# Performance work log

Hardware: AMD Instinct MI355X
Metric: run time of the kernel (lower is better)

The kernel has to match this reference:

```python
import jax, jax.numpy as jnp
import numpy as np

EMBED_DIM = 1024
NUM_HEADS = 16
HEAD_DIM = EMBED_DIM // NUM_HEADS


def setup_inputs() -> dict:
    key = jax.random.key(0)
    ks = jax.random.split(key, 9)
    s = 1.0 / np.sqrt(EMBED_DIM)
    inp = {"x": jax.random.normal(ks[0], (4, 8192, EMBED_DIM), dtype=jnp.float32)}
    for i, name in enumerate(["q", "k", "v", "o"]):
        inp[f"W{name}"] = jax.random.uniform(ks[1 + 2 * i], (EMBED_DIM, EMBED_DIM), jnp.float32, -s, s)
        inp[f"b{name}"] = jax.random.uniform(ks[2 + 2 * i], (EMBED_DIM,), jnp.float32, -s, s)
    return inp


def _kernel_exp(x):
    # exp(x - max over last dim), matches torch exp kernel
    return jnp.exp(x - jnp.max(x, axis=-1, keepdims=True))


def reference(x, Wq, bq, Wk, bk, Wv, bv, Wo, bo):
    b, s, e = x.shape
    def proj(W, bias):
        # (b,s,e) -> (b,h,s,d)
        return (x @ W.T + bias).reshape(b, s, NUM_HEADS, HEAD_DIM).transpose(0, 2, 1, 3)
    q = proj(Wq, bq)
    k = proj(Wk, bk)
    v = proj(Wv, bv)
    q_kern = _kernel_exp(q)
    k_kern = _kernel_exp(k)
    # global KV reduction: kv[b,h,d,e'] = sum_s k_kern[b,h,s,d] v[b,h,s,e']
    kv = jnp.einsum('bhsd,bhse->bhde', k_kern, v)
    # denom[b,h,q] = sum_{s,d} q_kern[b,h,q,d] k_kern[b,h,s,d] = q_kern . k_sum
    k_sum = jnp.sum(k_kern, axis=2)  # (b,h,d)
    denom = jnp.einsum('bhqd,bhd->bhq', q_kern, k_sum) + 1e-6
    y = jnp.einsum('bhqd,bhde->bhqe', q_kern, kv) / denom[..., None]
    y = y.transpose(0, 2, 1, 3).reshape(b, s, e)
    return y @ Wo.T + bo
```

## Files before the change

### kernel.cpp

```cpp
#include <hip/hip_runtime.h>
#include <hip/hip_bf16.h>
#include <cstdint>
#include <cstddef>


#define B_ 4
#define S_ 8192
#define E_ 1024
#define H_ 16
#define D_ 64
#define M_ (B_ * S_)

typedef __attribute__((ext_vector_type(8))) short s16x8;
typedef __attribute__((ext_vector_type(4))) short s16x4;
typedef __attribute__((ext_vector_type(4))) float f32x4_t;

__device__ __forceinline__ float bf2f(unsigned short u) {
  union { unsigned int i; float f; } c; c.i = ((unsigned int)u) << 16; return c.f;
}
__device__ __forceinline__ short f2bf(float f) {
  __hip_bfloat16 h = __float2bfloat16(f);
  return *reinterpret_cast<short*>(&h);
}

__global__ __launch_bounds__(256) void f32_to_bf16(
    const float* __restrict__ in, unsigned short* __restrict__ out, long n8)
{
  const long i = (long)blockIdx.x * 256 + threadIdx.x;
  if (i >= n8) return;
  const float4 lo = *(const float4*)(in + i * 8);
  const float4 hi = *(const float4*)(in + i * 8 + 4);
  s16x8 v;
  v[0] = f2bf(lo.x); v[1] = f2bf(lo.y); v[2] = f2bf(lo.z); v[3] = f2bf(lo.w);
  v[4] = f2bf(hi.x); v[5] = f2bf(hi.y); v[6] = f2bf(hi.z); v[7] = f2bf(hi.w);
  *(s16x8*)(out + i * 8) = v;
}

__device__ __forceinline__ void gload_lds16(const void* g, void* l) {
  __builtin_amdgcn_global_load_lds(
      (const __attribute__((address_space(1))) void*)g,
      (__attribute__((address_space(3))) void*)l, 16, 0, 0);
}

template <bool OUT_BF16>
__global__ __launch_bounds__(256) void gemm_bf16(
    const unsigned short* __restrict__ Xb,
    const unsigned short* __restrict__ Wb,
    const float* __restrict__ bias,
    void* __restrict__ Cout,
    int M, int N, int K)
{
  __shared__ unsigned short Al[128 * 64];
  __shared__ unsigned short Bl[128 * 64];
  const int tid = threadIdx.x;
  const int lane = tid & 63, w = tid >> 6;
  const int nwg = gridDim.x;
  const int cpx = nwg >> 3;
  const int swz = (blockIdx.x & 7) * cpx + (blockIdx.x >> 3);
  const int ntx = N >> 7;
  const int m0 = (swz / ntx) << 7, n0 = (swz % ntx) << 7;
  const int wr = w >> 1, wc = w & 1;
  const int srow = lane >> 3;
  const int scol = (lane & 7) * 8;
  const int fr = lane & 15, fq = lane >> 4;

  f32x4_t acc[4][4];
  #pragma unroll
  for (int i = 0; i < 4; ++i)
    #pragma unroll
    for (int j = 0; j < 4; ++j) acc[i][j] = (f32x4_t){0.f, 0.f, 0.f, 0.f};

  for (int kt = 0; kt < K; kt += 64) {
    #pragma unroll
    for (int i = 0; i < 4; ++i) {
      const int c = w * 4 + i;
      const int row = c * 8 + srow;
      gload_lds16(Xb + (size_t)(m0 + row) * K + kt + scol, Al + c * 512);
      gload_lds16(Wb + (size_t)(n0 + row) * K + kt + scol, Bl + c * 512);
    }
    asm volatile("s_waitcnt vmcnt(0)" ::: "memory");
    __syncthreads();
    #pragma unroll
    for (int ks = 0; ks < 2; ++ks) {
      s16x8 a[4], b[4];
      #pragma unroll
      for (int mi = 0; mi < 4; ++mi)
        a[mi] = *(const s16x8*)(Al + (wr * 64 + mi * 16 + fr) * 64 + ks * 32 + fq * 8);
      #pragma unroll
      for (int ni = 0; ni < 4; ++ni)
        b[ni] = *(const s16x8*)(Bl + (wc * 64 + ni * 16 + fr) * 64 + ks * 32 + fq * 8);
      #pragma unroll
      for (int mi = 0; mi < 4; ++mi)
        #pragma unroll
        for (int ni = 0; ni < 4; ++ni)
          acc[mi][ni] = __builtin_amdgcn_mfma_f32_16x16x32_bf16(a[mi], b[ni], acc[mi][ni], 0, 0, 0);
    }
    __syncthreads();
  }

  #pragma unroll
  for (int ni = 0; ni < 4; ++ni) {
    const int col = n0 + wc * 64 + ni * 16 + fr;
    const float bcol = bias[col];
    #pragma unroll
    for (int mi = 0; mi < 4; ++mi)
      #pragma unroll
      for (int r = 0; r < 4; ++r) {
        const int row = m0 + wr * 64 + mi * 16 + fq * 4 + r;
        const float v = acc[mi][ni][r] + bcol;
        if (OUT_BF16)
          ((unsigned short*)Cout)[(size_t)row * N + col] = (unsigned short)f2bf(v);
        else
          ((float*)Cout)[(size_t)row * N + col] = v;
      }
  }
}

#define NCHUNK 16
#define CROWS (S_ / NCHUNK)
#define KVR 8

__global__ __launch_bounds__(256) void kv_partial(
    const unsigned short* __restrict__ Kb, const unsigned short* __restrict__ Vb,
    float* __restrict__ kv_part, float* __restrict__ ksum_part)
{
  const int chunk = blockIdx.x;
  const int bh = blockIdx.y;
  const int b = bh >> 4, h = bh & 15;
  const int tid = threadIdx.x;
  const int lane = tid & 63, wave = tid >> 6;
  const int tx = tid & 15, ty = tid >> 4;

  __shared__ float kl[KVR][64];
  __shared__ float vl[KVR][64];
  __shared__ float ksw[4][64];

  const size_t base = ((size_t)b * S_ + (size_t)chunk * CROWS) * E_ + h * D_;
  const unsigned short* kbase = Kb + base;
  const unsigned short* vbase = Vb + base;

  float acc[4][4] = {};
  float ksacc = 0.f;

  const int which = tid >> 7;
  const int l2 = tid & 127;
  const int lr = l2 >> 4;
  const int lc = (l2 & 15) * 4;

  for (int s = 0; s < CROWS; s += KVR) {
    {
      const unsigned short* src = which ? vbase : kbase;
      float* dst = which ? &vl[lr][lc] : &kl[lr][lc];
      const s16x4 raw = *(const s16x4*)(src + (size_t)(s + lr) * E_ + lc);
      dst[0] = bf2f((unsigned short)raw[0]);
      dst[1] = bf2f((unsigned short)raw[1]);
      dst[2] = bf2f((unsigned short)raw[2]);
      dst[3] = bf2f((unsigned short)raw[3]);
    }
    __syncthreads();
    #pragma unroll
    for (int rr = 0; rr < 2; ++rr) {
      const int r = wave * 2 + rr;
      const float kx = kl[r][lane];
      float mx = kx;
      #pragma unroll
      for (int off = 32; off >= 1; off >>= 1) mx = fmaxf(mx, __shfl_xor(mx, off, 64));
      const float e = expf(kx - mx);
      kl[r][lane] = e;
      ksacc += e;
    }
    __syncthreads();
    #pragma unroll
    for (int r = 0; r < KVR; ++r) {
      const float4 kd = *(const float4*)&kl[r][ty * 4];
      const float4 ve = *(const float4*)&vl[r][tx * 4];
      const float kda[4] = {kd.x, kd.y, kd.z, kd.w};
      const float vea[4] = {ve.x, ve.y, ve.z, ve.w};
      #pragma unroll
      for (int i = 0; i < 4; ++i)
        #pragma unroll
        for (int j = 0; j < 4; ++j)
          acc[i][j] = fmaf(kda[i], vea[j], acc[i][j]);
    }
    __syncthreads();
  }

  const size_t pbase = ((size_t)bh * NCHUNK + chunk) * (D_ * D_);
  #pragma unroll
  for (int i = 0; i < 4; ++i) {
    float4 o = make_float4(acc[i][0], acc[i][1], acc[i][2], acc[i][3]);
    *(float4*)(kv_part + pbase + (size_t)(ty * 4 + i) * D_ + tx * 4) = o;
  }
  ksw[wave][lane] = ksacc;
  __syncthreads();
  if (wave == 0) {
    const float s = ksw[0][lane] + ksw[1][lane] + ksw[2][lane] + ksw[3][lane];
    ksum_part[((size_t)bh * NCHUNK + chunk) * D_ + lane] = s;
  }
}

__global__ __launch_bounds__(256) void kv_reduce(
    const float* __restrict__ kv_part, const float* __restrict__ ksum_part,
    float* __restrict__ kv, float* __restrict__ ksum)
{
  const int bh = blockIdx.x;
  const int tid = threadIdx.x;
  #pragma unroll
  for (int i = 0; i < 16; ++i) {
    const int e = tid + i * 256;
    float s = 0.f;
    #pragma unroll
    for (int c = 0; c < NCHUNK; ++c)
      s += kv_part[((size_t)bh * NCHUNK + c) * 4096 + e];
    kv[(size_t)bh * 4096 + e] = s;
  }
  if (tid < 64) {
    float s = 0.f;
    #pragma unroll
    for (int c = 0; c < NCHUNK; ++c)
      s += ksum_part[((size_t)bh * NCHUNK + c) * 64 + tid];
    ksum[(size_t)bh * 64 + tid] = s;
  }
}

__global__ __launch_bounds__(256) void y_kernel(
    const unsigned short* __restrict__ Qb, const float* __restrict__ kv,
    const float* __restrict__ ksum, unsigned short* __restrict__ Yb)
{
  const int tile = blockIdx.x;
  const int bh = blockIdx.y;
  const int b = bh >> 4, h = bh & 15;
  const int tid = threadIdx.x;
  const int lane = tid & 63, wave = tid >> 6;
  const int tx = tid & 15, ty = tid >> 4;

  __shared__ float qT[64][65];
  __shared__ float kvl[64][64];
  __shared__ float ksl[64];
  __shared__ float dinv[64];

  #pragma unroll
  for (int i = 0; i < 4; ++i) {
    const int l = tid + i * 256;
    *(float4*)&((float*)kvl)[4 * l] = *(const float4*)(kv + (size_t)bh * 4096 + 4 * l);
  }
  if (tid < 64) ksl[tid] = ksum[(size_t)bh * 64 + tid];
  __syncthreads();

  const unsigned short* qbase = Qb + ((size_t)b * S_ + (size_t)tile * 64) * E_ + h * D_;
  for (int rr = 0; rr < 16; ++rr) {
    const int r = wave * 16 + rr;
    const float q = bf2f(qbase[(size_t)r * E_ + lane]);
    float mx = q;
    #pragma unroll
    for (int off = 32; off >= 1; off >>= 1) mx = fmaxf(mx, __shfl_xor(mx, off, 64));
    const float e = expf(q - mx);
    qT[lane][r] = e;
    float dp = e * ksl[lane];
    #pragma unroll
    for (int off = 32; off >= 1; off >>= 1) dp += __shfl_xor(dp, off, 64);
    if (lane == 0) dinv[r] = 1.f / (dp + 1e-6f);
  }
  __syncthreads();

  float acc[4][4] = {};
  #pragma unroll 8
  for (int kk = 0; kk < 64; ++kk) {
    const float4 a = *(const float4*)&qT[kk][ty * 4];
    const float4 v = *(const float4*)&kvl[kk][tx * 4];
    const float aa[4] = {a.x, a.y, a.z, a.w};
    const float vv[4] = {v.x, v.y, v.z, v.w};
    #pragma unroll
    for (int i = 0; i < 4; ++i)
      #pragma unroll
      for (int j = 0; j < 4; ++j)
        acc[i][j] = fmaf(aa[i], vv[j], acc[i][j]);
  }

  unsigned short* ybase = Yb + ((size_t)b * S_ + (size_t)tile * 64) * E_ + h * D_;
  #pragma unroll
  for (int i = 0; i < 4; ++i) {
    const int r = ty * 4 + i;
    const float sc = dinv[r];
    s16x4 o;
    o[0] = f2bf(acc[i][0] * sc); o[1] = f2bf(acc[i][1] * sc);
    o[2] = f2bf(acc[i][2] * sc); o[3] = f2bf(acc[i][3] * sc);
    *(s16x4*)(ybase + (size_t)r * E_ + tx * 4) = o;
  }
}

extern "C" void kernel_launch(void* const* d_in, const int* in_sizes, int n_in,
                              void* d_out, int out_size, void* d_ws, size_t ws_size,
                              hipStream_t stream)
{
  (void)in_sizes; (void)n_in; (void)out_size; (void)ws_size;
  const float* x  = (const float*)d_in[0];
  const float* Wq = (const float*)d_in[1];
  const float* bq = (const float*)d_in[2];
  const float* Wk = (const float*)d_in[3];
  const float* bk = (const float*)d_in[4];
  const float* Wv = (const float*)d_in[5];
  const float* bv = (const float*)d_in[6];
  const float* Wo = (const float*)d_in[7];
  const float* bo = (const float*)d_in[8];
  float* out = (float*)d_out;

  const size_t ME = (size_t)M_ * E_;
  const size_t EE = (size_t)E_ * E_;
  unsigned short* qb  = (unsigned short*)d_ws;
  unsigned short* kb  = qb + ME;
  unsigned short* vb  = kb + ME;
  unsigned short* xb  = vb + ME;
  unsigned short* wqb = xb + ME;
  unsigned short* wkb = wqb + EE;
  unsigned short* wvb = wkb + EE;
  unsigned short* wob = wvb + EE;
  float* kv_part  = (float*)(wob + EE);
  float* ksum_prt = kv_part + (size_t)64 * NCHUNK * 4096;
  float* kvb      = ksum_prt + (size_t)64 * NCHUNK * 64;
  float* ksum     = kvb + (size_t)64 * 4096;
  unsigned short* yb = xb;

  f32_to_bf16<<<(int)(ME / 8 / 256), 256, 0, stream>>>(x, xb, (long)(ME / 8));
  f32_to_bf16<<<(int)(EE / 8 / 256), 256, 0, stream>>>(Wq, wqb, (long)(EE / 8));
  f32_to_bf16<<<(int)(EE / 8 / 256), 256, 0, stream>>>(Wk, wkb, (long)(EE / 8));
  f32_to_bf16<<<(int)(EE / 8 / 256), 256, 0, stream>>>(Wv, wvb, (long)(EE / 8));
  f32_to_bf16<<<(int)(EE / 8 / 256), 256, 0, stream>>>(Wo, wob, (long)(EE / 8));

  const int nwg = (M_ / 128) * (E_ / 128);
  gemm_bf16<true><<<nwg, 256, 0, stream>>>(xb, wqb, bq, qb, M_, E_, E_);
  gemm_bf16<true><<<nwg, 256, 0, stream>>>(xb, wkb, bk, kb, M_, E_, E_);
  gemm_bf16<true><<<nwg, 256, 0, stream>>>(xb, wvb, bv, vb, M_, E_, E_);
  kv_partial<<<dim3(NCHUNK, 64), 256, 0, stream>>>(kb, vb, kv_part, ksum_prt);
  kv_reduce<<<dim3(64), 256, 0, stream>>>(kv_part, ksum_prt, kvb, ksum);
  y_kernel<<<dim3(S_ / 64, 64), 256, 0, stream>>>(qb, kvb, ksum, yb);
  gemm_bf16<false><<<nwg, 256, 0, stream>>>(yb, wob, bo, out, M_, E_, E_);
}
```

Measured before the change: 956.5 us.

## Fuse QKV GEMMs with exp epilogue, restage KV reduction, use MFMA for output

Merges the three projection GEMMs into one launch over a concatenated weight matrix. The per-head max/exp feature map for Q and K now runs in the GEMM epilogue, so the later kernels read exp'd values directly. The KV partial kernel stages 64-row tiles and drops its per-row exp, and the y kernel replaces its scalar FMA loop with bf16 MFMA against a transposed bf16 KV matrix. In exchange, the KV matrix is rounded to bf16, which adds precision loss.

```diff
diff --git a/kernel.cpp b/kernel.cpp
--- a/kernel.cpp
+++ b/kernel.cpp
@@ -42,14 +42,15 @@
       (__attribute__((address_space(3))) void*)l, 16, 0, 0);
 }
 
-template <bool OUT_BF16>
-__global__ __launch_bounds__(256) void gemm_bf16(
+__global__ __launch_bounds__(256) void gemm_qkv(
     const unsigned short* __restrict__ Xb,
-    const unsigned short* __restrict__ Wb,
-    const float* __restrict__ bias,
-    void* __restrict__ Cout,
-    int M, int N, int K)
-{
+    const unsigned short* __restrict__ Wcat,
+    const float* __restrict__ bq, const float* __restrict__ bk,
+    const float* __restrict__ bv,
+    unsigned short* __restrict__ qe, unsigned short* __restrict__ ke,
+    unsigned short* __restrict__ vb)
+{
+  const int K = E_, N = 3 * E_;
   __shared__ unsigned short Al[128 * 64];
   __shared__ unsigned short Bl[128 * 64];
   const int tid = threadIdx.x;
@@ -76,7 +77,7 @@
       const int c = w * 4 + i;
       const int row = c * 8 + srow;
       gload_lds16(Xb + (size_t)(m0 + row) * K + kt + scol, Al + c * 512);
-      gload_lds16(Wb + (size_t)(n0 + row) * K + kt + scol, Bl + c * 512);
+      gload_lds16(Wcat + (size_t)(n0 + row) * K + kt + scol, Bl + c * 512);
     }
     asm volatile("s_waitcnt vmcnt(0)" ::: "memory");
     __syncthreads();
@@ -98,82 +99,97 @@
     __syncthreads();
   }
 
+  const int c0 = n0 + wc * 64;
+  const int id = c0 >> 10;
+  const int lc0 = c0 & 1023;
+  const float* bias = (id == 0) ? bq : (id == 1) ? bk : bv;
+  unsigned short* outp = (id == 0) ? qe : (id == 1) ? ke : vb;
+
+  float val[4][4][4];
   #pragma unroll
   for (int ni = 0; ni < 4; ++ni) {
-    const int col = n0 + wc * 64 + ni * 16 + fr;
-    const float bcol = bias[col];
+    const float bcol = bias[lc0 + ni * 16 + fr];
+    #pragma unroll
+    for (int mi = 0; mi < 4; ++mi)
+      #pragma unroll
+      for (int r = 0; r < 4; ++r)
+        val[mi][ni][r] = acc[mi][ni][r] + bcol;
+  }
+
+  if (id < 2) {
+    #pragma unroll
+    for (int mi = 0; mi < 4; ++mi)
+      #pragma unroll
+      for (int r = 0; r < 4; ++r) {
+        float mx = fmaxf(fmaxf(val[mi][0][r], val[mi][1][r]),
+                         fmaxf(val[mi][2][r], val[mi][3][r]));
+        mx = fmaxf(mx, __shfl_xor(mx, 1));
+        mx = fmaxf(mx, __shfl_xor(mx, 2));
+        mx = fmaxf(mx, __shfl_xor(mx, 4));
+        mx = fmaxf(mx, __shfl_xor(mx, 8));
+        #pragma unroll
+        for (int ni = 0; ni < 4; ++ni)
+          val[mi][ni][r] = expf(val[mi][ni][r] - mx);
+      }
+  }
+
+  #pragma unroll
+  for (int ni = 0; ni < 4; ++ni) {
+    const int col = lc0 + ni * 16 + fr;
     #pragma unroll
     for (int mi = 0; mi < 4; ++mi)
       #pragma unroll
       for (int r = 0; r < 4; ++r) {
         const int row = m0 + wr * 64 + mi * 16 + fq * 4 + r;
-        const float v = acc[mi][ni][r] + bcol;
-        if (OUT_BF16)
-          ((unsigned short*)Cout)[(size_t)row * N + col] = (unsigned short)f2bf(v);
-        else
-          ((float*)Cout)[(size_t)row * N + col] = v;
+        outp[(size_t)row * E_ + col] = (unsigned short)f2bf(val[mi][ni][r]);
       }
   }
 }
 
 #define NCHUNK 16
 #define CROWS (S_ / NCHUNK)
-#define KVR 8
-
-__global__ __launch_bounds__(256) void kv_partial(
-    const unsigned short* __restrict__ Kb, const unsigned short* __restrict__ Vb,
+
+__global__ __launch_bounds__(256) void kv_core(
+    const unsigned short* __restrict__ Ke, const unsigned short* __restrict__ Vb,
     float* __restrict__ kv_part, float* __restrict__ ksum_part)
 {
   const int chunk = blockIdx.x;
   const int bh = blockIdx.y;
   const int b = bh >> 4, h = bh & 15;
   const int tid = threadIdx.x;
-  const int lane = tid & 63, wave = tid >> 6;
   const int tx = tid & 15, ty = tid >> 4;
 
-  __shared__ float kl[KVR][64];
-  __shared__ float vl[KVR][64];
-  __shared__ float ksw[4][64];
-
-  const size_t base = ((size_t)b * S_ + (size_t)chunk * CROWS) * E_ + h * D_;
-  const unsigned short* kbase = Kb + base;
-  const unsigned short* vbase = Vb + base;
+  __shared__ float kst[64][64];
+  __shared__ float vst[64][64];
+
+  const size_t rbase = ((size_t)b * S_ + (size_t)chunk * CROWS);
 
   float acc[4][4] = {};
-  float ksacc = 0.f;
-
-  const int which = tid >> 7;
-  const int l2 = tid & 127;
-  const int lr = l2 >> 4;
-  const int lc = (l2 & 15) * 4;
-
-  for (int s = 0; s < CROWS; s += KVR) {
+  float ksacc[4] = {0.f, 0.f, 0.f, 0.f};
+
+  const int lrow = tid >> 2;
+  const int lcq = (tid & 3) * 16;
+
+  for (int it = 0; it < CROWS / 64; ++it) {
     {
-      const unsigned short* src = which ? vbase : kbase;
-      float* dst = which ? &vl[lr][lc] : &kl[lr][lc];
-      const s16x4 raw = *(const s16x4*)(src + (size_t)(s + lr) * E_ + lc);
-      dst[0] = bf2f((unsigned short)raw[0]);
-      dst[1] = bf2f((unsigned short)raw[1]);
-      dst[2] = bf2f((unsigned short)raw[2]);
-      dst[3] = bf2f((unsigned short)raw[3]);
-    }
-    __syncthreads();
-    #pragma unroll
-    for (int rr = 0; rr < 2; ++rr) {
-      const int r = wave * 2 + rr;
-      const float kx = kl[r][lane];
-      float mx = kx;
-      #pragma unroll
-      for (int off = 32; off >= 1; off >>= 1) mx = fmaxf(mx, __shfl_xor(mx, off, 64));
-      const float e = expf(kx - mx);
-      kl[r][lane] = e;
-      ksacc += e;
-    }
-    __syncthreads();
-    #pragma unroll
-    for (int r = 0; r < KVR; ++r) {
-      const float4 kd = *(const float4*)&kl[r][ty * 4];
-      const float4 ve = *(const float4*)&vl[r][tx * 4];
+      const size_t g = (rbase + it * 64 + lrow) * E_ + h * D_ + lcq;
+      const s16x8 k0 = *(const s16x8*)(Ke + g);
+      const s16x8 k1 = *(const s16x8*)(Ke + g + 8);
+      const s16x8 v0 = *(const s16x8*)(Vb + g);
+      const s16x8 v1 = *(const s16x8*)(Vb + g + 8);
+      #pragma unroll
+      for (int j = 0; j < 8; ++j) {
+        kst[lrow][lcq + j] = bf2f((unsigned short)k0[j]);
+        kst[lrow][lcq + 8 + j] = bf2f((unsigned short)k1[j]);
+        vst[lrow][lcq + j] = bf2f((unsigned short)v0[j]);
+        vst[lrow][lcq + 8 + j] = bf2f((unsigned short)v1[j]);
+      }
+    }
+    __syncthreads();
+    #pragma unroll 8
+    for (int s = 0; s < 64; ++s) {
+      const float4 kd = *(const float4*)&kst[s][ty * 4];
+      const float4 ve = *(const float4*)&vst[s][tx * 4];
       const float kda[4] = {kd.x, kd.y, kd.z, kd.w};
       const float vea[4] = {ve.x, ve.y, ve.z, ve.w};
       #pragma unroll
@@ -181,6 +197,10 @@
         #pragma unroll
         for (int j = 0; j < 4; ++j)
           acc[i][j] = fmaf(kda[i], vea[j], acc[i][j]);
+      if (tx == 0) {
+        #pragma unroll
+        for (int i = 0; i < 4; ++i) ksacc[i] += kda[i];
+      }
     }
     __syncthreads();
   }
@@ -191,28 +211,28 @@
     float4 o = make_float4(acc[i][0], acc[i][1], acc[i][2], acc[i][3]);
     *(float4*)(kv_part + pbase + (size_t)(ty * 4 + i) * D_ + tx * 4) = o;
   }
-  ksw[wave][lane] = ksacc;
-  __syncthreads();
-  if (wave == 0) {
-    const float s = ksw[0][lane] + ksw[1][lane] + ksw[2][lane] + ksw[3][lane];
-    ksum_part[((size_t)bh * NCHUNK + chunk) * D_ + lane] = s;
+  if (tx == 0) {
+    #pragma unroll
+    for (int i = 0; i < 4; ++i)
+      ksum_part[((size_t)bh * NCHUNK + chunk) * D_ + ty * 4 + i] = ksacc[i];
   }
 }
 
 __global__ __launch_bounds__(256) void kv_reduce(
     const float* __restrict__ kv_part, const float* __restrict__ ksum_part,
-    float* __restrict__ kv, float* __restrict__ ksum)
+    unsigned short* __restrict__ kvT, float* __restrict__ ksum)
 {
   const int bh = blockIdx.x;
   const int tid = threadIdx.x;
   #pragma unroll
   for (int i = 0; i < 16; ++i) {
-    const int e = tid + i * 256;
+    const int l = tid + i * 256;
+    const int d = l >> 6, e = l & 63;
     float s = 0.f;
     #pragma unroll
     for (int c = 0; c < NCHUNK; ++c)
-      s += kv_part[((size_t)bh * NCHUNK + c) * 4096 + e];
-    kv[(size_t)bh * 4096 + e] = s;
+      s += kv_part[((size_t)bh * NCHUNK + c) * 4096 + l];
+    kvT[(size_t)bh * 4096 + e * 64 + d] = (unsigned short)f2bf(s);
   }
   if (tid < 64) {
     float s = 0.f;
@@ -223,69 +243,133 @@
   }
 }
 
-__global__ __launch_bounds__(256) void y_kernel(
-    const unsigned short* __restrict__ Qb, const float* __restrict__ kv,
+__global__ __launch_bounds__(256) void y_mfma(
+    const unsigned short* __restrict__ Qe, const unsigned short* __restrict__ kvT,
     const float* __restrict__ ksum, unsigned short* __restrict__ Yb)
 {
   const int tile = blockIdx.x;
   const int bh = blockIdx.y;
   const int b = bh >> 4, h = bh & 15;
   const int tid = threadIdx.x;
-  const int lane = tid & 63, wave = tid >> 6;
-  const int tx = tid & 15, ty = tid >> 4;
-
-  __shared__ float qT[64][65];
-  __shared__ float kvl[64][64];
-  __shared__ float ksl[64];
-  __shared__ float dinv[64];
-
-  #pragma unroll
-  for (int i = 0; i < 4; ++i) {
-    const int l = tid + i * 256;
-    *(float4*)&((float*)kvl)[4 * l] = *(const float4*)(kv + (size_t)bh * 4096 + 4 * l);
-  }
-  if (tid < 64) ksl[tid] = ksum[(size_t)bh * 64 + tid];
-  __syncthreads();
-
-  const unsigned short* qbase = Qb + ((size_t)b * S_ + (size_t)tile * 64) * E_ + h * D_;
-  for (int rr = 0; rr < 16; ++rr) {
-    const int r = wave * 16 + rr;
-    const float q = bf2f(qbase[(size_t)r * E_ + lane]);
-    float mx = q;
-    #pragma unroll
-    for (int off = 32; off >= 1; off >>= 1) mx = fmaxf(mx, __shfl_xor(mx, off, 64));
-    const float e = expf(q - mx);
-    qT[lane][r] = e;
-    float dp = e * ksl[lane];
-    #pragma unroll
-    for (int off = 32; off >= 1; off >>= 1) dp += __shfl_xor(dp, off, 64);
-    if (lane == 0) dinv[r] = 1.f / (dp + 1e-6f);
-  }
-  __syncthreads();
-
-  float acc[4][4] = {};
-  #pragma unroll 8
-  for (int kk = 0; kk < 64; ++kk) {
-    const float4 a = *(const float4*)&qT[kk][ty * 4];
-    const float4 v = *(const float4*)&kvl[kk][tx * 4];
-    const float aa[4] = {a.x, a.y, a.z, a.w};
-    const float vv[4] = {v.x, v.y, v.z, v.w};
-    #pragma unroll
-    for (int i = 0; i < 4; ++i)
-      #pragma unroll
-      for (int j = 0; j < 4; ++j)
-        acc[i][j] = fmaf(aa[i], vv[j], acc[i][j]);
-  }
-
-  unsigned short* ybase = Yb + ((size_t)b * S_ + (size_t)tile * 64) * E_ + h * D_;
-  #pragma unroll
-  for (int i = 0; i < 4; ++i) {
-    const int r = ty * 4 + i;
-    const float sc = dinv[r];
-    s16x4 o;
-    o[0] = f2bf(acc[i][0] * sc); o[1] = f2bf(acc[i][1] * sc);
-    o[2] = f2bf(acc[i][2] * sc); o[3] = f2bf(acc[i][3] * sc);
-    *(s16x4*)(ybase + (size_t)r * E_ + tx * 4) = o;
+  const int lane = tid & 63, w = tid >> 6;
+  const int fr = lane & 15, fq = lane >> 4;
+
+  s16x8 bf[4][2];
+  const unsigned short* kvb = kvT + (size_t)bh * 4096;
+  #pragma unroll
+  for (int ni = 0; ni < 4; ++ni)
+    #pragma unroll
+    for (int ks = 0; ks < 2; ++ks)
+      bf[ni][ks] = *(const s16x8*)(kvb + (ni * 16 + fr) * 64 + ks * 32 + fq * 8);
+
+  float ks0[8], ks1[8];
+  {
+    const float* kp = ksum + (size_t)bh * 64;
+    *(float4*)&ks0[0] = *(const float4*)(kp + fq * 8);
+    *(float4*)&ks0[4] = *(const float4*)(kp + fq * 8 + 4);
+    *(float4*)&ks1[0] = *(const float4*)(kp + 32 + fq * 8);
+    *(float4*)&ks1[4] = *(const float4*)(kp + 32 + fq * 8 + 4);
+  }
+
+  const size_t srow = (size_t)b * S_ + (size_t)tile * 64 + w * 16 + fr;
+  const unsigned short* qrow = Qe + srow * E_ + h * D_;
+  const s16x8 a0 = *(const s16x8*)(qrow + fq * 8);
+  const s16x8 a1 = *(const s16x8*)(qrow + 32 + fq * 8);
+
+  float dp = 0.f;
+  #pragma unroll
+  for (int j = 0; j < 8; ++j) {
+    dp = fmaf(bf2f((unsigned short)a0[j]), ks0[j], dp);
+    dp = fmaf(bf2f((unsigned short)a1[j]), ks1[j], dp);
+  }
+  dp += __shfl_xor(dp, 16);
+  dp += __shfl_xor(dp, 32);
+  const float dinv = 1.f / (dp + 1e-6f);
+
+  f32x4_t acc[4];
+  #pragma unroll
+  for (int ni = 0; ni < 4; ++ni) {
+    acc[ni] = (f32x4_t){0.f, 0.f, 0.f, 0.f};
+    acc[ni] = __builtin_amdgcn_mfma_f32_16x16x32_bf16(a0, bf[ni][0], acc[ni], 0, 0, 0);
+    acc[ni] = __builtin_amdgcn_mfma_f32_16x16x32_bf16(a1, bf[ni][1], acc[ni], 0, 0, 0);
+  }
+
+  unsigned short* ybase = Yb + ((size_t)b * S_ + (size_t)tile * 64 + w * 16) * E_ + h * D_;
+  #pragma unroll
+  for (int r = 0; r < 4; ++r) {
+    const int lrow = fq * 4 + r;
+    const float di = __shfl(dinv, lrow);
+    #pragma unroll
+    for (int ni = 0; ni < 4; ++ni)
+      ybase[(size_t)lrow * E_ + ni * 16 + fr] = (unsigned short)f2bf(acc[ni][r] * di);
+  }
+}
+
+__global__ __launch_bounds__(256) void gemm_o(
+    const unsigned short* __restrict__ Xb,
+    const unsigned short* __restrict__ Wb,
+    const float* __restrict__ bias,
+    float* __restrict__ C, int M, int N, int K)
+{
+  __shared__ unsigned short Al[128 * 64];
+  __shared__ unsigned short Bl[128 * 64];
+  const int tid = threadIdx.x;
+  const int lane = tid & 63, w = tid >> 6;
+  const int nwg = gridDim.x;
+  const int cpx = nwg >> 3;
+  const int swz = (blockIdx.x & 7) * cpx + (blockIdx.x >> 3);
+  const int ntx = N >> 7;
+  const int m0 = (swz / ntx) << 7, n0 = (swz % ntx) << 7;
+  const int wr = w >> 1, wc = w & 1;
+  const int srow = lane >> 3;
+  const int scol = (lane & 7) * 8;
+  const int fr = lane & 15, fq = lane >> 4;
+
+  f32x4_t acc[4][4];
+  #pragma unroll
+  for (int i = 0; i < 4; ++i)
+    #pragma unroll
+    for (int j = 0; j < 4; ++j) acc[i][j] = (f32x4_t){0.f, 0.f, 0.f, 0.f};
+
+  for (int kt = 0; kt < K; kt += 64) {
+    #pragma unroll
+    for (int i = 0; i < 4; ++i) {
+      const int c = w * 4 + i;
+      const int row = c * 8 + srow;
+      gload_lds16(Xb + (size_t)(m0 + row) * K + kt + scol, Al + c * 512);
+      gload_lds16(Wb + (size_t)(n0 + row) * K + kt + scol, Bl + c * 512);
+    }
+    asm volatile("s_waitcnt vmcnt(0)" ::: "memory");
+    __syncthreads();
+    #pragma unroll
+    for (int ks = 0; ks < 2; ++ks) {
+      s16x8 a[4], b[4];
+      #pragma unroll
+      for (int mi = 0; mi < 4; ++mi)
+        a[mi] = *(const s16x8*)(Al + (wr * 64 + mi * 16 + fr) * 64 + ks * 32 + fq * 8);
+      #pragma unroll
+      for (int ni = 0; ni < 4; ++ni)
+        b[ni] = *(const s16x8*)(Bl + (wc * 64 + ni * 16 + fr) * 64 + ks * 32 + fq * 8);
+      #pragma unroll
+      for (int mi = 0; mi < 4; ++mi)
+        #pragma unroll
+        for (int ni = 0; ni < 4; ++ni)
+          acc[mi][ni] = __builtin_amdgcn_mfma_f32_16x16x32_bf16(a[mi], b[ni], acc[mi][ni], 0, 0, 0);
+    }
+    __syncthreads();
+  }
+
+  #pragma unroll
+  for (int ni = 0; ni < 4; ++ni) {
+    const int col = n0 + wc * 64 + ni * 16 + fr;
+    const float bcol = bias[col];
+    #pragma unroll
+    for (int mi = 0; mi < 4; ++mi)
+      #pragma unroll
+      for (int r = 0; r < 4; ++r) {
+        const int row = m0 + wr * 64 + mi * 16 + fq * 4 + r;
+        C[(size_t)row * N + col] = acc[mi][ni][r] + bcol;
+      }
   }
 }
 
@@ -307,32 +391,28 @@
 
   const size_t ME = (size_t)M_ * E_;
   const size_t EE = (size_t)E_ * E_;
-  unsigned short* qb  = (unsigned short*)d_ws;
-  unsigned short* kb  = qb + ME;
-  unsigned short* vb  = kb + ME;
-  unsigned short* xb  = vb + ME;
-  unsigned short* wqb = xb + ME;
-  unsigned short* wkb = wqb + EE;
-  unsigned short* wvb = wkb + EE;
-  unsigned short* wob = wvb + EE;
+  unsigned short* xb   = (unsigned short*)d_ws;
+  unsigned short* qe   = xb + ME;
+  unsigned short* ke   = qe + ME;
+  unsigned short* vb   = ke + ME;
+  unsigned short* wqkv = vb + ME;
+  unsigned short* wob  = wqkv + 3 * EE;
   float* kv_part  = (float*)(wob + EE);
   float* ksum_prt = kv_part + (size_t)64 * NCHUNK * 4096;
-  float* kvb      = ksum_prt + (size_t)64 * NCHUNK * 64;
-  float* ksum     = kvb + (size_t)64 * 4096;
-  unsigned short* yb = xb;
+  unsigned short* kvT = (unsigned short*)(ksum_prt + (size_t)64 * NCHUNK * 64);
+  float* ksum = (float*)(kvT + (size_t)64 * 4096);
+  unsigned short* yb = ke;
 
   f32_to_bf16<<<(int)(ME / 8 / 256), 256, 0, stream>>>(x, xb, (long)(ME / 8));
-  f32_to_bf16<<<(int)(EE / 8 / 256), 256, 0, stream>>>(Wq, wqb, (long)(EE / 8));
-  f32_to_bf16<<<(int)(EE / 8 / 256), 256, 0, stream>>>(Wk, wkb, (long)(EE / 8));
-  f32_to_bf16<<<(int)(EE / 8 / 256), 256, 0, stream>>>(Wv, wvb, (long)(EE / 8));
+  f32_to_bf16<<<(int)(EE / 8 / 256), 256, 0, stream>>>(Wq, wqkv, (long)(EE / 8));
+  f32_to_bf16<<<(int)(EE / 8 / 256), 256, 0, stream>>>(Wk, wqkv + EE, (long)(EE / 8));
+  f32_to_bf16<<<(int)(EE / 8 / 256), 256, 0, stream>>>(Wv, wqkv + 2 * EE, (long)(EE / 8));
   f32_to_bf16<<<(int)(EE / 8 / 256), 256, 0, stream>>>(Wo, wob, (long)(EE / 8));
 
-  const int nwg = (M_ / 128) * (E_ / 128);
-  gemm_bf16<true><<<nwg, 256, 0, stream>>>(xb, wqb, bq, qb, M_, E_, E_);
-  gemm_bf16<true><<<nwg, 256, 0, stream>>>(xb, wkb, bk, kb, M_, E_, E_);
-  gemm_bf16<true><<<nwg, 256, 0, stream>>>(xb, wvb, bv, vb, M_, E_, E_);
-  kv_partial<<<dim3(NCHUNK, 64), 256, 0, stream>>>(kb, vb, kv_part, ksum_prt);
-  kv_reduce<<<dim3(64), 256, 0, stream>>>(kv_part, ksum_prt, kvb, ksum);
-  y_kernel<<<dim3(S_ / 64, 64), 256, 0, stream>>>(qb, kvb, ksum, yb);
-  gemm_bf16<false><<<nwg, 256, 0, stream>>>(yb, wob, bo, out, M_, E_, E_);
-}
+  gemm_qkv<<<(M_ / 128) * (3 * E_ / 128), 256, 0, stream>>>(
+      xb, wqkv, bq, bk, bv, qe, ke, vb);
+  kv_core<<<dim3(NCHUNK, 64), 256, 0, stream>>>(ke, vb, kv_part, ksum_prt);
+  kv_reduce<<<dim3(64), 256, 0, stream>>>(kv_part, ksum_prt, kvT, ksum);
+  y_mfma<<<dim3(S_ / 64, 64), 256, 0, stream>>>(qe, kvT, ksum, yb);
+  gemm_o<<<(M_ / 128) * (E_ / 128), 256, 0, stream>>>(yb, wob, bo, out, M_, E_, E_);
+}
```

Result: faster. 858.7 us (-10.2%).
